# Kernel optimization log

Measured on AMD Instinct MI355X. Metric: run time of the kernel, lower is better.

Reference implementation:

```python
import jax, jax.numpy as jnp
import numpy as np

N_NODES = 100000
EPS = 1e-5


def gcn_conv(x, edge_index, W, b):
    # PyG GCNConv: add self loops, symmetric normalization, aggregate at target.
    n = x.shape[0]
    xw = x @ W                                  # [N, F_out]
    loop = jnp.arange(n)
    src = jnp.concatenate([edge_index[0], loop])
    dst = jnp.concatenate([edge_index[1], loop])
    deg = jax.ops.segment_sum(jnp.ones_like(dst, dtype=xw.dtype), dst, num_segments=n)
    dinv = jnp.where(deg > 0, jax.lax.rsqrt(deg), 0.0)
    norm = dinv[src] * dinv[dst]                # [E+N]
    out = jax.ops.segment_sum(norm[:, None] * xw[src], dst, num_segments=n)
    return out + b


def batch_norm(x, gamma, beta):
    # training-mode BatchNorm1d over node dim
    m = x.mean(axis=0)
    v = x.var(axis=0)
    return (x - m) * jax.lax.rsqrt(v + EPS) * gamma + beta


def setup_inputs() -> dict:
    key = jax.random.key(0)
    ks = jax.random.split(key, 16)
    dims = [(128, 256), (256, 128), (128, 64)]
    inp = {
        "x": jax.random.normal(ks[0], (N_NODES, 128), dtype=jnp.float32),
        "edge_index": jax.random.randint(ks[1], (2, 1600000), 0, N_NODES),
        "pos_edge_index": jax.random.randint(ks[2], (2, 200000), 0, N_NODES),
        "neg_edge_index": jax.random.randint(ks[3], (2, 200000), 0, N_NODES),
    }
    for i, (fi, fo) in enumerate(dims, start=1):
        inp[f"W{i}"] = jax.random.normal(ks[3 + i], (fi, fo), dtype=jnp.float32) / np.sqrt(fi)
        inp[f"b{i}"] = jnp.zeros((fo,), dtype=jnp.float32)
        inp[f"g{i}"] = jnp.ones((fo,), dtype=jnp.float32)
        inp[f"beta{i}"] = jnp.zeros((fo,), dtype=jnp.float32)
    return inp


def reference(x, edge_index, pos_edge_index, neg_edge_index,
              W1, b1, g1, beta1, W2, b2, g2, beta2, W3, b3, g3, beta3):
    # encode
    h = gcn_conv(x, edge_index, W1, b1)
    h = jax.nn.sigmoid(batch_norm(h, g1, beta1))
    h = gcn_conv(h, edge_index, W2, b2)
    h = jax.nn.sigmoid(batch_norm(h, g2, beta2))
    h = gcn_conv(h, edge_index, W3, b3)
    z = batch_norm(h, g3, beta3)                # [N, 64]
    # decode
    ei = jnp.concatenate([pos_edge_index, neg_edge_index], axis=-1)
    logits = jnp.sum(z[ei[0]] * z[ei[1]], axis=-1)
    return logits
```

## Files before the change

### kernel.cpp

```cpp
#include <hip/hip_runtime.h>
#include <hip/hip_bf16.h>
#include <stddef.h>


#define WAVE 64
#define BSHIFT 9
#define SCHUNK 4096

typedef __attribute__((ext_vector_type(8))) short short8;
typedef __attribute__((ext_vector_type(4))) float f32x4;

__device__ __forceinline__ float bl(uint g) { return __uint_as_float(g << 16); }
__device__ __forceinline__ float bh(uint g) { return __uint_as_float(g & 0xffff0000u); }
__device__ __forceinline__ ushort f2b(float f) {
    uint u = __float_as_uint(f);
    return (ushort)((u + 0x7fffu + ((u >> 16) & 1u)) >> 16);
}
__device__ __forceinline__ uint pack2(float lo, float hi) {
    return (uint)f2b(lo) | ((uint)f2b(hi) << 16);
}

__global__ __launch_bounds__(256) void k_bhist(const int* __restrict__ dst, int* __restrict__ gh, int E) {
    __shared__ int lh[256];
    lh[threadIdx.x] = 0; __syncthreads();
    int i = blockIdx.x * 256 + threadIdx.x, stride = gridDim.x * 256;
    for (; i < E; i += stride) atomicAdd(&lh[dst[i] >> BSHIFT], 1);
    __syncthreads();
    int v = lh[threadIdx.x];
    if (v) atomicAdd(&gh[threadIdx.x], v);
}

__global__ void k_bscan(const int* __restrict__ gh, int* __restrict__ boff, int* __restrict__ bcur) {
    __shared__ int ls[256];
    int t = threadIdx.x;
    int v = gh[t];
    ls[t] = v; __syncthreads();
    for (int off = 1; off < 256; off <<= 1) {
        int x = (t >= off) ? ls[t - off] : 0;
        __syncthreads();
        ls[t] += x;
        __syncthreads();
    }
    int excl = ls[t] - v;
    boff[t] = excl; bcur[t] = excl;
    if (t == 255) boff[256] = ls[255];
}

__global__ __launch_bounds__(256) void k_bscatter(const int* __restrict__ src, const int* __restrict__ dst,
                                                  int* __restrict__ gcur, uint* __restrict__ pairs, int E) {
    __shared__ int lh[256];
    int t = threadIdx.x;
    int base = blockIdx.x * SCHUNK;
    lh[t] = 0; __syncthreads();
    int rs[16], rd[16];
    #pragma unroll
    for (int i = 0; i < 16; ++i) {
        int idx = base + i * 256 + t;
        if (idx < E) { rs[i] = src[idx]; rd[i] = dst[idx]; atomicAdd(&lh[rd[i] >> BSHIFT], 1); }
        else rd[i] = -1;
    }
    __syncthreads();
    int cnt_b = lh[t];
    int b0 = cnt_b ? atomicAdd(&gcur[t], cnt_b) : 0;
    lh[t] = b0;
    __syncthreads();
    #pragma unroll
    for (int i = 0; i < 16; ++i) {
        if (rd[i] >= 0) {
            int p = atomicAdd(&lh[rd[i] >> BSHIFT], 1);
            pairs[p] = ((uint)(rd[i] & 511) << 17) | (uint)rs[i];
        }
    }
}

__global__ __launch_bounds__(256) void k_bfine(const uint* __restrict__ pairs, const int* __restrict__ boff,
                                               int* __restrict__ rowptr, int* __restrict__ srcs,
                                               float* __restrict__ dinv, int N, int E) {
    __shared__ int lcnt[512];
    __shared__ int ls[256];
    int b = blockIdx.x, t = threadIdx.x;
    int d0 = b << BSHIFT;
    int e0 = boff[b], e1 = boff[b + 1];
    lcnt[t] = 0; lcnt[t + 256] = 0;
    __syncthreads();
    for (int e = e0 + t; e < e1; e += 256)
        atomicAdd(&lcnt[pairs[e] >> 17], 1);
    __syncthreads();
    int c0 = lcnt[2 * t], c1 = lcnt[2 * t + 1];
    ls[t] = c0 + c1;
    __syncthreads();
    for (int off = 1; off < 256; off <<= 1) {
        int x = (t >= off) ? ls[t - off] : 0;
        __syncthreads();
        ls[t] += x;
        __syncthreads();
    }
    int excl = ls[t] - (c0 + c1);
    int s0 = excl, s1 = excl + c0;
    int d = d0 + 2 * t;
    if (d < N)     { rowptr[d] = e0 + s0;     dinv[d] = rsqrtf((float)(c0 + 1)); }
    if (d + 1 < N) { rowptr[d + 1] = e0 + s1; dinv[d + 1] = rsqrtf((float)(c1 + 1)); }
    if (b == 0 && t == 0) rowptr[N] = E;
    lcnt[2 * t] = s0; lcnt[2 * t + 1] = s1;
    __syncthreads();
    for (int e = e0 + t; e < e1; e += 256) {
        uint p = pairs[e];
        int pos = atomicAdd(&lcnt[p >> 17], 1);
        srcs[e0 + pos] = (int)(p & 0x1FFFFu);
    }
}

__global__ void k_convx(const float* __restrict__ in, ushort* __restrict__ out, size_t n4) {
    size_t i = (size_t)blockIdx.x * blockDim.x + threadIdx.x;
    if (i >= n4) return;
    float4 v = reinterpret_cast<const float4*>(in)[i];
    uint2 o;
    o.x = pack2(v.x, v.y);
    o.y = pack2(v.z, v.w);
    reinterpret_cast<uint2*>(out)[i] = o;
}

__global__ void k_convW(const float* __restrict__ W1, const float* __restrict__ W2,
                        const float* __restrict__ W3, ushort* __restrict__ Wt1,
                        ushort* __restrict__ Wt2, ushort* __restrict__ Wt3) {
    int i = blockIdx.x * blockDim.x + threadIdx.x;
    const float* W; ushort* Wt; int K, Nn, j;
    if (i < 32768)      { W = W1; Wt = Wt1; K = 128; Nn = 256; j = i; }
    else if (i < 65536) { W = W2; Wt = Wt2; K = 256; Nn = 128; j = i - 32768; }
    else if (i < 73728) { W = W3; Wt = Wt3; K = 128; Nn = 64;  j = i - 65536; }
    else return;
    int k = j / Nn, n = j % Nn;
    Wt[(size_t)n * K + k] = f2b(W[k * Nn + n]);
}

template<int F>
__global__ __launch_bounds__(256) void k_agg(const ushort* __restrict__ in, ushort* __restrict__ out,
                                             const int* __restrict__ rowptr, const int* __restrict__ srcs,
                                             const float* __restrict__ dinv, int N) {
    constexpr int L = (F * 2) / 16;
    int wv = threadIdx.x >> 6, lane = threadIdx.x & 63;
    int node = (blockIdx.x * 4 + wv) * (64 / L) + lane / L;
    int sl = lane % L;
    if (node >= N) return;
    const uint4* inq = reinterpret_cast<const uint4*>(in);
    float di = dinv[node];
    float acc[8];
    {
        uint4 v = inq[(size_t)node * L + sl];
        acc[0] = di * bl(v.x); acc[1] = di * bh(v.x);
        acc[2] = di * bl(v.y); acc[3] = di * bh(v.y);
        acc[4] = di * bl(v.z); acc[5] = di * bh(v.z);
        acc[6] = di * bl(v.w); acc[7] = di * bh(v.w);
    }
    int e = rowptr[node], e1 = rowptr[node + 1];
    for (; e + 3 < e1; e += 4) {
        int s0 = srcs[e], s1 = srcs[e + 1], s2 = srcs[e + 2], s3 = srcs[e + 3];
        float d0 = dinv[s0], d1 = dinv[s1], d2 = dinv[s2], d3 = dinv[s3];
        uint4 v0 = inq[(size_t)s0 * L + sl];
        uint4 v1 = inq[(size_t)s1 * L + sl];
        uint4 v2 = inq[(size_t)s2 * L + sl];
        uint4 v3 = inq[(size_t)s3 * L + sl];
        acc[0] += d0 * bl(v0.x) + d1 * bl(v1.x) + d2 * bl(v2.x) + d3 * bl(v3.x);
        acc[1] += d0 * bh(v0.x) + d1 * bh(v1.x) + d2 * bh(v2.x) + d3 * bh(v3.x);
        acc[2] += d0 * bl(v0.y) + d1 * bl(v1.y) + d2 * bl(v2.y) + d3 * bl(v3.y);
        acc[3] += d0 * bh(v0.y) + d1 * bh(v1.y) + d2 * bh(v2.y) + d3 * bh(v3.y);
        acc[4] += d0 * bl(v0.z) + d1 * bl(v1.z) + d2 * bl(v2.z) + d3 * bl(v3.z);
        acc[5] += d0 * bh(v0.z) + d1 * bh(v1.z) + d2 * bh(v2.z) + d3 * bh(v3.z);
        acc[6] += d0 * bl(v0.w) + d1 * bl(v1.w) + d2 * bl(v2.w) + d3 * bl(v3.w);
        acc[7] += d0 * bh(v0.w) + d1 * bh(v1.w) + d2 * bh(v2.w) + d3 * bh(v3.w);
    }
    for (; e < e1; ++e) {
        int s0 = srcs[e];
        float d0 = dinv[s0];
        uint4 v0 = inq[(size_t)s0 * L + sl];
        acc[0] += d0 * bl(v0.x); acc[1] += d0 * bh(v0.x);
        acc[2] += d0 * bl(v0.y); acc[3] += d0 * bh(v0.y);
        acc[4] += d0 * bl(v0.z); acc[5] += d0 * bh(v0.z);
        acc[6] += d0 * bl(v0.w); acc[7] += d0 * bh(v0.w);
    }
    uint4 o;
    o.x = pack2(acc[0] * di, acc[1] * di);
    o.y = pack2(acc[2] * di, acc[3] * di);
    o.z = pack2(acc[4] * di, acc[5] * di);
    o.w = pack2(acc[6] * di, acc[7] * di);
    reinterpret_cast<uint4*>(out)[(size_t)node * L + sl] = o;
}

template<int F>
__global__ __launch_bounds__(256) void k_bnstats(const ushort* __restrict__ h, float* __restrict__ gsum,
                                                 float* __restrict__ gsq, int N) {
    constexpr int C = F / 8;
    constexpr int RPW = 64 / C;
    __shared__ float ls[4][16][16];
    int wv = threadIdx.x >> 6, lane = threadIdx.x & 63;
    int fidx = lane % C, rsub = lane / C;
    int row = (blockIdx.x * 4 + wv) * RPW + rsub;
    int rstride = gridDim.x * 4 * RPW;
    const uint4* hq = reinterpret_cast<const uint4*>(h);
    float s[8] = {}, q[8] = {};
    for (int r = row; r < N; r += rstride) {
        uint4 v = hq[(size_t)r * C + fidx];
        float x;
        x = bl(v.x); s[0] += x; q[0] += x * x;
        x = bh(v.x); s[1] += x; q[1] += x * x;
        x = bl(v.y); s[2] += x; q[2] += x * x;
        x = bh(v.y); s[3] += x; q[3] += x * x;
        x = bl(v.z); s[4] += x; q[4] += x * x;
        x = bh(v.z); s[5] += x; q[5] += x * x;
        x = bl(v.w); s[6] += x; q[6] += x * x;
        x = bh(v.w); s[7] += x; q[7] += x * x;
    }
    #pragma unroll
    for (int m = C; m < 64; m <<= 1) {
        #pragma unroll
        for (int j = 0; j < 8; ++j) { s[j] += __shfl_xor(s[j], m); q[j] += __shfl_xor(q[j], m); }
    }
    if (lane < C) {
        #pragma unroll
        for (int j = 0; j < 8; ++j) { ls[wv][lane][j] = s[j]; ls[wv][lane][8 + j] = q[j]; }
    }
    __syncthreads();
    int t = threadIdx.x;
    if (t < F) {
        int ch = t / 8, j = t % 8;
        float S = 0.f, Q = 0.f;
        #pragma unroll
        for (int w = 0; w < 4; ++w) { S += ls[w][ch][j]; Q += ls[w][ch][8 + j]; }
        atomicAdd(&gsum[t], S); atomicAdd(&gsq[t], Q);
    }
}

template<int K, int NF, int NPASS, bool APPLY, bool STATS>
__global__ __launch_bounds__(256) void k_mfma(const ushort* __restrict__ A, const ushort* __restrict__ Wt,
                                              ushort* __restrict__ C, int M, int Nout,
                                              const float* __restrict__ bsum, const float* __restrict__ bsq,
                                              const float* __restrict__ bg, const float* __restrict__ bb,
                                              float invN,
                                              float* __restrict__ gsum, float* __restrict__ gsq) {
    constexpr int CH = K / 8;
    constexpr int KS = K / 32;
    __shared__ uint4 Alds[128 * CH];
    __shared__ float scl[APPLY ? K : 1], shl[APPLY ? K : 1];
    int m0 = blockIdx.x * 128;
    int t = threadIdx.x;
    int w = t >> 6, lane = t & 63;
    int wr = w >> 1, wc = w & 1;
    int rf = lane & 15, kg = lane >> 4;

    if constexpr (APPLY) {
        for (int i = t; i < K; i += 256) {
            float m = bsum[i] * invN;
            float var = bsq[i] * invN - m * m;
            float sc = bg[i] * rsqrtf(var + 1e-5f);
            scl[i] = sc; shl[i] = bb[i] - m * sc;
        }
        __syncthreads();
    }

    #pragma unroll
    for (int i = 0; i < CH / 2; ++i) {
        int chunk = i * 256 + t;
        int r = chunk / CH, c = chunk % CH;
        int gr = m0 + r; if (gr >= M) gr = M - 1;
        uint4 v = *reinterpret_cast<const uint4*>(A + (size_t)gr * K + c * 8);
        if constexpr (APPLY) {
            uint u[4] = {v.x, v.y, v.z, v.w};
            int kb = c * 8;
            #pragma unroll
            for (int j = 0; j < 4; ++j) {
                int k = kb + 2 * j;
                float x0 = bl(u[j]) * scl[k] + shl[k];
                float x1 = bh(u[j]) * scl[k + 1] + shl[k + 1];
                x0 = 1.f / (1.f + __expf(-x0));
                x1 = 1.f / (1.f + __expf(-x1));
                u[j] = pack2(x0, x1);
            }
            v.x = u[0]; v.y = u[1]; v.z = u[2]; v.w = u[3];
        }
        Alds[r * CH + (c ^ (r & 7))] = v;
    }
    __syncthreads();

    for (int pass = 0; pass < NPASS; ++pass) {
        int n0 = pass * NF * 32;
        const ushort* bp[NF];
        #pragma unroll
        for (int nf = 0; nf < NF; ++nf)
            bp[nf] = Wt + (size_t)(n0 + wc * (NF * 16) + nf * 16 + rf) * K + kg * 8;

        f32x4 acc[4][NF];
        #pragma unroll
        for (int mf = 0; mf < 4; ++mf)
            #pragma unroll
            for (int nf = 0; nf < NF; ++nf)
                acc[mf][nf] = (f32x4){0.f, 0.f, 0.f, 0.f};

        short8 bcur[NF];
        #pragma unroll
        for (int nf = 0; nf < NF; ++nf)
            bcur[nf] = *reinterpret_cast<const short8*>(bp[nf]);

        for (int ks = 0; ks < KS; ++ks) {
            short8 bnxt[NF];
            if (ks + 1 < KS) {
                #pragma unroll
                for (int nf = 0; nf < NF; ++nf)
                    bnxt[nf] = *reinterpret_cast<const short8*>(bp[nf] + (ks + 1) * 32);
            } else {
                #pragma unroll
                for (int nf = 0; nf < NF; ++nf) bnxt[nf] = bcur[nf];
            }
            short8 a[4];
            #pragma unroll
            for (int mf = 0; mf < 4; ++mf) {
                int R = wr * 64 + mf * 16 + rf;
                int c = ks * 4 + kg;
                a[mf] = *reinterpret_cast<const short8*>(&Alds[R * CH + (c ^ (R & 7))]);
            }
            #pragma unroll
            for (int mf = 0; mf < 4; ++mf)
                #pragma unroll
                for (int nf = 0; nf < NF; ++nf)
                    acc[mf][nf] = __builtin_amdgcn_mfma_f32_16x16x32_bf16(a[mf], bcur[nf], acc[mf][nf], 0, 0, 0);
            #pragma unroll
            for (int nf = 0; nf < NF; ++nf) bcur[nf] = bnxt[nf];
        }

        #pragma unroll
        for (int mf = 0; mf < 4; ++mf)
            #pragma unroll
            for (int nf = 0; nf < NF; ++nf) {
                int col = n0 + wc * (NF * 16) + nf * 16 + rf;
                #pragma unroll
                for (int j = 0; j < 4; ++j) {
                    int row = m0 + wr * 64 + mf * 16 + kg * 4 + j;
                    if (row < M) C[(size_t)row * Nout + col] = f2b(acc[mf][nf][j]);
                }
            }

        if constexpr (STATS) {
            __shared__ float bns[2][NF * 32], bnq[2][NF * 32];
            __syncthreads();
            #pragma unroll
            for (int nf = 0; nf < NF; ++nf) {
                float cs = 0.f, cq = 0.f;
                #pragma unroll
                for (int mf = 0; mf < 4; ++mf)
                    #pragma unroll
                    for (int j = 0; j < 4; ++j) {
                        int row = m0 + wr * 64 + mf * 16 + kg * 4 + j;
                        float v = (row < M) ? acc[mf][nf][j] : 0.f;
                        cs += v; cq += v * v;
                    }
                cs += __shfl_xor(cs, 16); cs += __shfl_xor(cs, 32);
                cq += __shfl_xor(cq, 16); cq += __shfl_xor(cq, 32);
                if (kg == 0) { bns[wr][wc * (NF * 16) + nf * 16 + rf] = cs; bnq[wr][wc * (NF * 16) + nf * 16 + rf] = cq; }
            }
            __syncthreads();
            if (t < NF * 32) {
                atomicAdd(&gsum[n0 + t], bns[0][t] + bns[1][t]);
                atomicAdd(&gsq[n0 + t],  bnq[0][t] + bnq[1][t]);
            }
        }
    }
}

__global__ __launch_bounds__(256) void k_decode(const ushort* __restrict__ h,
                                                const float* __restrict__ bsum, const float* __restrict__ bsq,
                                                const float* __restrict__ bg, const float* __restrict__ bb,
                                                float invN,
                                                const int* __restrict__ pos, const int* __restrict__ neg,
                                                int Pp, int Pn, float* __restrict__ out) {
    __shared__ float scl[64], shl[64];
    int t = threadIdx.x;
    if (t < 64) {
        float m = bsum[t] * invN;
        float var = bsq[t] * invN - m * m;
        float sc = bg[t] * rsqrtf(var + 1e-5f);
        scl[t] = sc; shl[t] = bb[t] - m * sc;
    }
    __syncthreads();
    int gid = blockIdx.x * 16 + (t >> 4);
    int l = t & 15;
    int P = Pp + Pn;
    if (gid >= P) return;
    int a, b;
    if (gid < Pp) { a = pos[gid]; b = pos[Pp + gid]; }
    else          { int e = gid - Pp; a = neg[e]; b = neg[Pn + e]; }
    const uint2* hu = reinterpret_cast<const uint2*>(h);
    uint2 ua = hu[(size_t)a * 16 + l];
    uint2 ub = hu[(size_t)b * 16 + l];
    int f = l * 4;
    float s0 = scl[f], s1 = scl[f + 1], s2 = scl[f + 2], s3 = scl[f + 3];
    float t0 = shl[f], t1 = shl[f + 1], t2 = shl[f + 2], t3 = shl[f + 3];
    float a0 = bl(ua.x) * s0 + t0, a1 = bh(ua.x) * s1 + t1, a2 = bl(ua.y) * s2 + t2, a3 = bh(ua.y) * s3 + t3;
    float b0 = bl(ub.x) * s0 + t0, b1 = bh(ub.x) * s1 + t1, b2 = bl(ub.y) * s2 + t2, b3 = bh(ub.y) * s3 + t3;
    float d = a0 * b0 + a1 * b1 + a2 * b2 + a3 * b3;
    d += __shfl_xor(d, 1);
    d += __shfl_xor(d, 2);
    d += __shfl_xor(d, 4);
    d += __shfl_xor(d, 8);
    if (l == 0) out[gid] = d;
}

extern "C" void kernel_launch(void* const* d_in, const int* in_sizes, int n_in,
                              void* d_out, int out_size, void* d_ws, size_t ws_size,
                              hipStream_t stream) {
    const float* x   = (const float*)d_in[0];
    const int*   ei  = (const int*)d_in[1];
    const int*   pe  = (const int*)d_in[2];
    const int*   ne  = (const int*)d_in[3];
    const float* W1  = (const float*)d_in[4];
    const float* g1  = (const float*)d_in[6];
    const float* be1 = (const float*)d_in[7];
    const float* W2  = (const float*)d_in[8];
    const float* g2  = (const float*)d_in[10];
    const float* be2 = (const float*)d_in[11];
    const float* W3  = (const float*)d_in[12];
    const float* g3  = (const float*)d_in[14];
    const float* be3 = (const float*)d_in[15];
    float* out = (float*)d_out;

    const int N  = in_sizes[0] / 128;
    const int E  = in_sizes[1] / 2;
    const int Pp = in_sizes[2] / 2;
    const int Pn = in_sizes[3] / 2;
    const float invN = 1.0f / (float)N;

    char* ws = (char*)d_ws;
    auto carve = [&](size_t bytes) -> char* {
        char* p = ws;
        ws += (bytes + 255) & ~(size_t)255;
        return p;
    };
    char*  zz     = carve(256 * 4 + 896 * 4);
    int*   gh     = (int*)zz;
    float* sums1  = (float*)(zz + 1024);
    float* sq1    = sums1 + 256;
    float* sums2  = sq1 + 256;
    float* sq2    = sums2 + 128;
    float* sums3  = sq2 + 128;
    float* sq3    = sums3 + 64;
    size_t zz_bytes = 1024 + 896 * 4;

    int*    boff   = (int*)carve(257 * 4);
    int*    bcur   = (int*)carve(256 * 4);
    int*    rowptr = (int*)carve((size_t)(N + 1) * 4);
    float*  dinv   = (float*)carve((size_t)N * 4);
    int*    srcs   = (int*)carve((size_t)E * 4);
    uint*   pairs  = (uint*)carve((size_t)E * 4);
    ushort* Wt1    = (ushort*)carve(128 * 256 * 2);
    ushort* Wt2    = (ushort*)carve(256 * 128 * 2);
    ushort* Wt3    = (ushort*)carve(128 * 64 * 2);
    ushort* b1     = (ushort*)carve((size_t)N * 128 * 2);
    ushort* b2     = (ushort*)carve((size_t)N * 128 * 2);
    ushort* b3     = (ushort*)carve((size_t)N * 256 * 2);

    const int* e_src = ei;
    const int* e_dst = ei + E;
    const int NBUCK = (N + (1 << BSHIFT) - 1) >> BSHIFT;

    hipMemsetAsync(zz, 0, zz_bytes, stream);

    k_bhist<<<2048, 256, 0, stream>>>(e_dst, gh, E);
    k_bscan<<<1, 256, 0, stream>>>(gh, boff, bcur);
    k_bscatter<<<(E + SCHUNK - 1) / SCHUNK, 256, 0, stream>>>(e_src, e_dst, bcur, pairs, E);
    k_bfine<<<NBUCK, 256, 0, stream>>>(pairs, boff, rowptr, srcs, dinv, N, E);

    {
        size_t n4 = (size_t)N * 128 / 4;
        k_convx<<<(int)((n4 + 255) / 256), 256, 0, stream>>>(x, b1, n4);
        k_convW<<<288, 256, 0, stream>>>(W1, W2, W3, Wt1, Wt2, Wt3);
    }

    const int mblk = (N + 127) / 128;
    const int agg128 = (N + 15) / 16;
    const int agg64  = (N + 31) / 32;

    k_agg<128><<<agg128, 256, 0, stream>>>(b1, b2, rowptr, srcs, dinv, N);
    k_mfma<128, 4, 2, false, true><<<mblk, 256, 0, stream>>>(b2, Wt1, b3, N, 256,
        nullptr, nullptr, nullptr, nullptr, invN, sums1, sq1);

    k_mfma<256, 4, 1, true, false><<<mblk, 256, 0, stream>>>(b3, Wt2, b1, N, 128,
        sums1, sq1, g1, be1, invN, nullptr, nullptr);
    k_agg<128><<<agg128, 256, 0, stream>>>(b1, b2, rowptr, srcs, dinv, N);
    k_bnstats<128><<<512, 256, 0, stream>>>(b2, sums2, sq2, N);

    k_mfma<128, 2, 1, true, false><<<mblk, 256, 0, stream>>>(b2, Wt3, b1, N, 64,
        sums2, sq2, g2, be2, invN, nullptr, nullptr);
    k_agg<64><<<agg64, 256, 0, stream>>>(b1, b2, rowptr, srcs, dinv, N);
    k_bnstats<64><<<512, 256, 0, stream>>>(b2, sums3, sq3, N);

    k_decode<<<(Pp + Pn + 15) / 16, 256, 0, stream>>>(b2, sums3, sq3, g3, be3, invN,
                                                      pe, ne, Pp, Pn, out);
}
```

Baseline: 563.7 us.

## Split BN-sigmoid apply into separate kernel and stage GEMM A via global_load_lds

Moves the batch-norm plus sigmoid applied to GEMM inputs out of the MFMA kernel into a standalone in-place elementwise kernel. The GEMM kernel then loads A tiles directly into LDS with global_load_lds in 64-wide K steps, double-buffered, instead of going through registers. This is meant to cut VGPR traffic and overlap loads with MFMA work. In exchange it adds an extra full read and write pass over the activations for each apply, plus two more launches.

Result: faster. 544.4 us (-3.4%).

```diff
diff --git a/kernel.cpp b/kernel.cpp
--- a/kernel.cpp
+++ b/kernel.cpp
@@ -18,6 +18,12 @@
 }
 __device__ __forceinline__ uint pack2(float lo, float hi) {
     return (uint)f2b(lo) | ((uint)f2b(hi) << 16);
+}
+
+__device__ __forceinline__ void gload16(const ushort* g, ushort* l) {
+    __builtin_amdgcn_global_load_lds(
+        (const __attribute__((address_space(1))) uint*)g,
+        (__attribute__((address_space(3))) uint*)l, 16, 0, 0);
 }
 
 __global__ __launch_bounds__(256) void k_bhist(const int* __restrict__ dst, int* __restrict__ gh, int E) {
@@ -230,56 +236,64 @@
     }
 }
 
-template<int K, int NF, int NPASS, bool APPLY, bool STATS>
-__global__ __launch_bounds__(256) void k_mfma(const ushort* __restrict__ A, const ushort* __restrict__ Wt,
+template<int F>
+__global__ __launch_bounds__(256) void k_apply(ushort* __restrict__ h,
+                                               const float* __restrict__ bsum, const float* __restrict__ bsq,
+                                               const float* __restrict__ bg, const float* __restrict__ bb,
+                                               float invN, long NT) {
+    constexpr int CPR = F / 8;
+    int tid = blockIdx.x * 256 + threadIdx.x;
+    int fb = (tid % CPR) * 8;
+    float sc[8], sh[8];
+    #pragma unroll
+    for (int j = 0; j < 8; ++j) {
+        float m = bsum[fb + j] * invN;
+        float var = bsq[fb + j] * invN - m * m;
+        float s = bg[fb + j] * rsqrtf(var + 1e-5f);
+        sc[j] = s; sh[j] = bb[fb + j] - m * s;
+    }
+    uint4* hq = reinterpret_cast<uint4*>(h);
+    long stride = (long)gridDim.x * 256;
+    for (long i = tid; i < NT; i += stride) {
+        uint4 v = hq[i];
+        float x[8];
+        x[0] = bl(v.x); x[1] = bh(v.x); x[2] = bl(v.y); x[3] = bh(v.y);
+        x[4] = bl(v.z); x[5] = bh(v.z); x[6] = bl(v.w); x[7] = bh(v.w);
+        #pragma unroll
+        for (int j = 0; j < 8; ++j) {
+            float y = x[j] * sc[j] + sh[j];
+            x[j] = 1.f / (1.f + __expf(-y));
+        }
+        v.x = pack2(x[0], x[1]); v.y = pack2(x[2], x[3]);
+        v.z = pack2(x[4], x[5]); v.w = pack2(x[6], x[7]);
+        hq[i] = v;
+    }
+}
+
+template<int K, int NF, int NPASS, bool STATS>
+__global__ __launch_bounds__(256) void k_gemm(const ushort* __restrict__ A, const ushort* __restrict__ Wt,
                                               ushort* __restrict__ C, int M, int Nout,
-                                              const float* __restrict__ bsum, const float* __restrict__ bsq,
-                                              const float* __restrict__ bg, const float* __restrict__ bb,
-                                              float invN,
                                               float* __restrict__ gsum, float* __restrict__ gsq) {
-    constexpr int CH = K / 8;
+    constexpr int S = K / 64;
     constexpr int KS = K / 32;
-    __shared__ uint4 Alds[128 * CH];
-    __shared__ float scl[APPLY ? K : 1], shl[APPLY ? K : 1];
+    __shared__ ushort Alds[2][128 * 64];
     int m0 = blockIdx.x * 128;
     int t = threadIdx.x;
     int w = t >> 6, lane = t & 63;
     int wr = w >> 1, wc = w & 1;
     int rf = lane & 15, kg = lane >> 4;
 
-    if constexpr (APPLY) {
-        for (int i = t; i < K; i += 256) {
-            float m = bsum[i] * invN;
-            float var = bsq[i] * invN - m * m;
-            float sc = bg[i] * rsqrtf(var + 1e-5f);
-            scl[i] = sc; shl[i] = bb[i] - m * sc;
+    auto stage = [&](int buf, int step) {
+        #pragma unroll
+        for (int i = 0; i < 4; ++i) {
+            int cb = (i * 4 + w) * 64;
+            int chunk = cb + lane;
+            int r = chunk >> 3, cs = chunk & 7;
+            int c = cs ^ (r & 7);
+            int gr = m0 + r; if (gr >= M) gr = M - 1;
+            gload16(A + (size_t)gr * K + step * 64 + c * 8, &Alds[buf][cb * 8]);
         }
-        __syncthreads();
-    }
-
-    #pragma unroll
-    for (int i = 0; i < CH / 2; ++i) {
-        int chunk = i * 256 + t;
-        int r = chunk / CH, c = chunk % CH;
-        int gr = m0 + r; if (gr >= M) gr = M - 1;
-        uint4 v = *reinterpret_cast<const uint4*>(A + (size_t)gr * K + c * 8);
-        if constexpr (APPLY) {
-            uint u[4] = {v.x, v.y, v.z, v.w};
-            int kb = c * 8;
-            #pragma unroll
-            for (int j = 0; j < 4; ++j) {
-                int k = kb + 2 * j;
-                float x0 = bl(u[j]) * scl[k] + shl[k];
-                float x1 = bh(u[j]) * scl[k + 1] + shl[k + 1];
-                x0 = 1.f / (1.f + __expf(-x0));
-                x1 = 1.f / (1.f + __expf(-x1));
-                u[j] = pack2(x0, x1);
-            }
-            v.x = u[0]; v.y = u[1]; v.z = u[2]; v.w = u[3];
-        }
-        Alds[r * CH + (c ^ (r & 7))] = v;
-    }
-    __syncthreads();
+    };
 
     for (int pass = 0; pass < NPASS; ++pass) {
         int n0 = pass * NF * 32;
@@ -295,35 +309,48 @@
             for (int nf = 0; nf < NF; ++nf)
                 acc[mf][nf] = (f32x4){0.f, 0.f, 0.f, 0.f};
 
+        if (pass == 0) {
+            stage(0, 0);
+            if constexpr (S == 2) stage(1, 1);
+            __syncthreads();
+        }
+
         short8 bcur[NF];
         #pragma unroll
         for (int nf = 0; nf < NF; ++nf)
             bcur[nf] = *reinterpret_cast<const short8*>(bp[nf]);
 
-        for (int ks = 0; ks < KS; ++ks) {
-            short8 bnxt[NF];
-            if (ks + 1 < KS) {
-                #pragma unroll
-                for (int nf = 0; nf < NF; ++nf)
-                    bnxt[nf] = *reinterpret_cast<const short8*>(bp[nf] + (ks + 1) * 32);
-            } else {
-                #pragma unroll
-                for (int nf = 0; nf < NF; ++nf) bnxt[nf] = bcur[nf];
-            }
-            short8 a[4];
-            #pragma unroll
-            for (int mf = 0; mf < 4; ++mf) {
-                int R = wr * 64 + mf * 16 + rf;
-                int c = ks * 4 + kg;
-                a[mf] = *reinterpret_cast<const short8*>(&Alds[R * CH + (c ^ (R & 7))]);
+        for (int s = 0; s < S; ++s) {
+            if constexpr (S > 2) {
+                if (s + 1 < S && pass == 0) stage((s + 1) & 1, s + 1);
             }
             #pragma unroll
-            for (int mf = 0; mf < 4; ++mf)
+            for (int ksl = 0; ksl < 2; ++ksl) {
+                int gs = s * 2 + ksl;
+                short8 bnxt[NF];
+                if (gs + 1 < KS) {
+                    #pragma unroll
+                    for (int nf = 0; nf < NF; ++nf)
+                        bnxt[nf] = *reinterpret_cast<const short8*>(bp[nf] + (gs + 1) * 32);
+                }
+                short8 a[4];
                 #pragma unroll
-                for (int nf = 0; nf < NF; ++nf)
-                    acc[mf][nf] = __builtin_amdgcn_mfma_f32_16x16x32_bf16(a[mf], bcur[nf], acc[mf][nf], 0, 0, 0);
-            #pragma unroll
-            for (int nf = 0; nf < NF; ++nf) bcur[nf] = bnxt[nf];
+                for (int mf = 0; mf < 4; ++mf) {
+                    int R = wr * 64 + mf * 16 + rf;
+                    int idx = R * 8 + ((ksl * 4 + kg) ^ (R & 7));
+                    a[mf] = *reinterpret_cast<const short8*>(&Alds[s & 1][idx * 8]);
+                }
+                #pragma unroll
+                for (int mf = 0; mf < 4; ++mf)
+                    #pragma unroll
+                    for (int nf = 0; nf < NF; ++nf)
+                        acc[mf][nf] = __builtin_amdgcn_mfma_f32_16x16x32_bf16(a[mf], bcur[nf], acc[mf][nf], 0, 0, 0);
+                if (gs + 1 < KS) {
+                    #pragma unroll
+                    for (int nf = 0; nf < NF; ++nf) bcur[nf] = bnxt[nf];
+                }
+            }
+            if constexpr (S > 2) __syncthreads();
         }
 
         #pragma unroll
@@ -478,16 +505,15 @@
     const int agg64  = (N + 31) / 32;
 
     k_agg<128><<<agg128, 256, 0, stream>>>(b1, b2, rowptr, srcs, dinv, N);
-    k_mfma<128, 4, 2, false, true><<<mblk, 256, 0, stream>>>(b2, Wt1, b3, N, 256,
-        nullptr, nullptr, nullptr, nullptr, invN, sums1, sq1);
-
-    k_mfma<256, 4, 1, true, false><<<mblk, 256, 0, stream>>>(b3, Wt2, b1, N, 128,
-        sums1, sq1, g1, be1, invN, nullptr, nullptr);
+    k_gemm<128, 4, 2, true><<<mblk, 256, 0, stream>>>(b2, Wt1, b3, N, 256, sums1, sq1);
+    k_apply<256><<<2048, 256, 0, stream>>>(b3, sums1, sq1, g1, be1, invN, (long)N * 32);
+
+    k_gemm<256, 4, 1, false><<<mblk, 256, 0, stream>>>(b3, Wt2, b1, N, 128, nullptr, nullptr);
     k_agg<128><<<agg128, 256, 0, stream>>>(b1, b2, rowptr, srcs, dinv, N);
     k_bnstats<128><<<512, 256, 0, stream>>>(b2, sums2, sq2, N);
-
-    k_mfma<128, 2, 1, true, false><<<mblk, 256, 0, stream>>>(b2, Wt3, b1, N, 64,
-        sums2, sq2, g2, be2, invN, nullptr, nullptr);
+    k_apply<128><<<2048, 256, 0, stream>>>(b2, sums2, sq2, g2, be2, invN, (long)N * 16);
+
+    k_gemm<128, 2, 1, false><<<mblk, 256, 0, stream>>>(b2, Wt3, b1, N, 64, nullptr, nullptr);
     k_agg<64><<<agg64, 256, 0, stream>>>(b1, b2, rowptr, srcs, dinv, N);
     k_bnstats<64><<<512, 256, 0, stream>>>(b2, sums3, sq3, N);
 
```
